# Kernel tuning notes

Hardware: AMD Instinct MI355X
Metric: run time of the kernel (lower is better)

The kernel has to match this reference:

```python
import jax
import jax.numpy as jnp
from jax import lax
import numpy as np

B = 65536
T = 1          # forced by x.view(B, -1) feeding Linear(40, 4)
IN = 1260
H = 40
OUT = 4


def setup_inputs() -> dict:
    key = jax.random.key(0)
    ks = jax.random.split(key, 16)
    s = 0.05
    inp = {"x": jax.random.normal(ks[0], (B, T, IN), dtype=jnp.float32)}
    # 3-layer LSTM params, torch gate order (i, f, g, o) stacked along dim 0
    dims_in = [IN, H, H]
    for l in range(3):
        inp[f"W_ih{l}"] = jax.random.normal(ks[1 + 4 * l], (4 * H, dims_in[l]), dtype=jnp.float32) * s
        inp[f"W_hh{l}"] = jax.random.normal(ks[2 + 4 * l], (4 * H, H), dtype=jnp.float32) * s
        inp[f"b_ih{l}"] = jax.random.normal(ks[3 + 4 * l], (4 * H,), dtype=jnp.float32) * s
        inp[f"b_hh{l}"] = jax.random.normal(ks[4 + 4 * l], (4 * H,), dtype=jnp.float32) * s
    inp["W_out"] = jax.random.normal(ks[13], (OUT, H), dtype=jnp.float32) * s
    inp["b_out"] = jax.random.normal(ks[14], (OUT,), dtype=jnp.float32) * s
    return inp


def _lstm_layer(x, W_ih, W_hh, b_ih, b_hh):
    # x: [B, T, D_in] -> [B, T, H]; zero initial (h, c) as in torch default
    b, _, _ = x.shape
    h0 = jnp.zeros((b, H), x.dtype)
    c0 = jnp.zeros((b, H), x.dtype)

    def step(carry, xt):
        h, c = carry
        gates = xt @ W_ih.T + b_ih + h @ W_hh.T + b_hh   # [B, 4H]
        i, f, g, o = jnp.split(gates, 4, axis=-1)
        i = jax.nn.sigmoid(i)
        f = jax.nn.sigmoid(f)
        g = jnp.tanh(g)
        o = jax.nn.sigmoid(o)
        c = f * c + i * g
        h = o * jnp.tanh(c)
        return (h, c), h

    _, ys = lax.scan(step, (h0, c0), jnp.swapaxes(x, 0, 1))  # ys: [T, B, H]
    return jnp.swapaxes(ys, 0, 1)


def reference(x, W_ih0, W_hh0, b_ih0, b_hh0,
              W_ih1, W_hh1, b_ih1, b_hh1,
              W_ih2, W_hh2, b_ih2, b_hh2,
              W_out, b_out):
    h = _lstm_layer(x, W_ih0, W_hh0, b_ih0, b_hh0)
    h = _lstm_layer(h, W_ih1, W_hh1, b_ih1, b_hh1)
    h = _lstm_layer(h, W_ih2, W_hh2, b_ih2, b_hh2)   # [B, T, H]
    flat = h.reshape(h.shape[0], -1)                  # [B, T*H] == [B, 40]
    return flat @ W_out.T + b_out                     # [B, 4]
```

## Files before the change

kernel.cpp:

```cpp
#include <hip/hip_runtime.h>

typedef float f32x4 __attribute__((ext_vector_type(4)));
typedef __bf16 bf16x8 __attribute__((ext_vector_type(8)));
typedef unsigned short u16x4 __attribute__((ext_vector_type(4)));
typedef unsigned int u32x4 __attribute__((ext_vector_type(4)));


__device__ __forceinline__ unsigned short f2bf(float f) {
  unsigned int u = __builtin_bit_cast(unsigned int, f);
  u = (u + 0x7FFFu + ((u >> 16) & 1u)) >> 16;
  return (unsigned short)u;
}
__device__ __forceinline__ float sigm(float v) { return 1.0f / (1.0f + __expf(-v)); }
__device__ __forceinline__ float tanh_(float v) { return 1.0f - 2.0f / (__expf(2.0f * v) + 1.0f); }

__device__ __forceinline__ int srow_of(int col) {
  return col + (col < 40 ? 0 : (col < 80 ? 40 : 80));
}

__global__ __launch_bounds__(256) void prep_kernel(
    const float* __restrict__ W_ih0, const float* __restrict__ b_ih0, const float* __restrict__ b_hh0,
    const float* __restrict__ W_ih1, const float* __restrict__ b_ih1, const float* __restrict__ b_hh1,
    const float* __restrict__ W_ih2, const float* __restrict__ b_ih2, const float* __restrict__ b_hh2,
    unsigned short* __restrict__ W0bf, unsigned short* __restrict__ W1bf,
    unsigned short* __restrict__ W2bf, float* __restrict__ bias)
{
  int idx = blockIdx.x * 256 + threadIdx.x;
  {
    int c = idx >> 13, rem = idx & 8191;
    int col = rem >> 6, kk = rem & 63;
    int k = (c << 6) + kk;
    unsigned short v = 0;
    if (col < 120 && k < 1260) v = f2bf(W_ih0[srow_of(col) * 1260 + k]);
    W0bf[(c << 13) + (col << 6) + (kk ^ ((col & 7) << 3))] = v;
  }
  if (idx < 8192) {
    int col = idx >> 6, kk = idx & 63;
    unsigned short v1 = 0, v2 = 0;
    if (col < 120 && kk < 40) {
      int sr = srow_of(col);
      v1 = f2bf(W_ih1[sr * 40 + kk]);
      v2 = f2bf(W_ih2[sr * 40 + kk]);
    }
    int d = (col << 6) + (kk ^ ((col & 7) << 3));
    W1bf[d] = v1;
    W2bf[d] = v2;
  }
  if (idx < 384) {
    int l = idx >> 7, col = idx & 127;
    float v = 0.0f;
    if (col < 120) {
      int sr = srow_of(col);
      v = (l == 0) ? (b_ih0[sr] + b_hh0[sr])
        : (l == 1) ? (b_ih1[sr] + b_hh1[sr])
                   : (b_ih2[sr] + b_hh2[sr]);
    }
    bias[idx] = v;
  }
}

__global__ __launch_bounds__(256, 2) void lstm_main(
    const float* __restrict__ x,
    const unsigned short* __restrict__ W0bf,
    const unsigned short* __restrict__ W1bf,
    const unsigned short* __restrict__ W2bf,
    const float* __restrict__ bias,
    const float* __restrict__ W_out,
    const float* __restrict__ b_out,
    float* __restrict__ out)
{
  __shared__ __align__(16) unsigned short Abuf[2][64 * 64];
  __shared__ __align__(16) unsigned short Wbuf[2][128 * 64];
  __shared__ __align__(16) float gates[64 * 124];

  const int tid = threadIdx.x;
  const int wave = tid >> 6;
  const int lane = tid & 63;
  const int l15 = lane & 15;
  const int l4 = lane >> 4;
  const long base_row = (long)blockIdx.x * 64;

  const int arow = tid >> 4;
  const int akq = tid & 15;
  const float* xbase = x + (base_row + arow) * 1260 + akq * 4;

  f32x4 acc[4][2];
  f32x4 areg[4];
  u32x4 wreg[4];
  const f32x4 zero4 = {0.0f, 0.0f, 0.0f, 0.0f};

  auto zacc = [&]() {
#pragma unroll
    for (int i = 0; i < 4; ++i)
#pragma unroll
      for (int j = 0; j < 2; ++j) acc[i][j] = zero4;
  };

  auto loadA = [&](int c) {
    int kg = (c << 6) + (akq << 2);
    bool v = (kg < 1257);
#pragma unroll
    for (int p = 0; p < 4; ++p) {
      const float* s = xbase + p * (16 * 1260) + (c << 6);
      areg[p] = v ? *(const f32x4*)s : zero4;
    }
  };

  auto storeA = [&](int b) {
#pragma unroll
    for (int p = 0; p < 4; ++p) {
      int row = (p << 4) + arow;
      int kk0 = akq << 2;
      int sidx = (row << 6) + (kk0 ^ ((row & 7) << 3));
      u16x4 pk;
      pk.x = f2bf(areg[p].x); pk.y = f2bf(areg[p].y);
      pk.z = f2bf(areg[p].z); pk.w = f2bf(areg[p].w);
      *(u16x4*)&Abuf[b][sidx] = pk;
    }
  };

  auto loadW = [&](const unsigned short* src) {
    const u32x4* ws = (const u32x4*)src;
#pragma unroll
    for (int j = 0; j < 4; ++j) wreg[j] = ws[j * 256 + tid];
  };

  auto storeW = [&](int b) {
    u32x4* wd = (u32x4*)&Wbuf[b][0];
#pragma unroll
    for (int j = 0; j < 4; ++j) wd[j * 256 + tid] = wreg[j];
  };

  auto compute = [&](int b) {
#pragma unroll
    for (int ks = 0; ks < 2; ++ks) {
      bf16x8 af[4], wf[2];
      int kk = (ks << 5) + (l4 << 3);
#pragma unroll
      for (int mt = 0; mt < 4; ++mt) {
        int row = (mt << 4) + l15;
        af[mt] = *(const bf16x8*)&Abuf[b][(row << 6) + (kk ^ ((row & 7) << 3))];
      }
#pragma unroll
      for (int ct = 0; ct < 2; ++ct) {
        int col = (wave << 5) + (ct << 4) + l15;
        wf[ct] = *(const bf16x8*)&Wbuf[b][(col << 6) + (kk ^ ((col & 7) << 3))];
      }
#pragma unroll
      for (int mt = 0; mt < 4; ++mt)
#pragma unroll
        for (int ct = 0; ct < 2; ++ct)
          acc[mt][ct] = __builtin_amdgcn_mfma_f32_16x16x32_bf16(af[mt], wf[ct], acc[mt][ct], 0, 0, 0);
    }
  };

  auto writegates = [&](const float* bp) {
#pragma unroll
    for (int ct = 0; ct < 2; ++ct) {
      int col = (wave << 5) + (ct << 4) + l15;
      if (col < 120) {
        float bv = bp[col];
#pragma unroll
        for (int mt = 0; mt < 4; ++mt) {
          int row = (mt << 4) + (l4 << 2);
#pragma unroll
          for (int r = 0; r < 4; ++r)
            gates[(row + r) * 124 + col] = acc[mt][ct][r] + bv;
        }
      }
    }
  };

  auto zeroA0 = [&]() {
    unsigned int* az = (unsigned int*)&Abuf[0][0];
#pragma unroll
    for (int j = 0; j < 8; ++j) az[j * 256 + tid] = 0u;
  };

  auto act_bf = [&]() {
#pragma unroll
    for (int it = 0; it < 10; ++it) {
      int idx = it * 256 + tid;
      int row = idx / 40;
      int h = idx - row * 40;
      const float* gr = &gates[row * 124];
      float i = sigm(gr[h]);
      float g = tanh_(gr[40 + h]);
      float o = sigm(gr[80 + h]);
      float hv = o * tanh_(i * g);
      Abuf[0][(row << 6) + (h ^ ((row & 7) << 3))] = f2bf(hv);
    }
  };

  zacc();
  loadA(0); loadW(W0bf);
  storeA(0); storeW(0);
  __syncthreads();
  for (int c = 0; c < 20; ++c) {
    int cur = c & 1;
    if (c < 19) { loadA(c + 1); loadW(W0bf + ((long)(c + 1) << 13)); }
    compute(cur);
    if (c < 19) { storeA(cur ^ 1); storeW(cur ^ 1); }
    __syncthreads();
  }

  writegates(bias);
  zeroA0();
  loadW(W1bf);
  __syncthreads();

  act_bf();
  storeW(0);
  __syncthreads();

  zacc();
  compute(0);
  __syncthreads();

  writegates(bias + 128);
  zeroA0();
  loadW(W2bf);
  __syncthreads();

  act_bf();
  storeW(0);
  __syncthreads();

  zacc();
  compute(0);
  __syncthreads();

  writegates(bias + 256);
  __syncthreads();

#pragma unroll
  for (int it = 0; it < 10; ++it) {
    int idx = it * 256 + tid;
    int row = idx / 40;
    int h = idx - row * 40;
    float* gr = &gates[row * 124];
    float i = sigm(gr[h]);
    float g = tanh_(gr[40 + h]);
    float o = sigm(gr[80 + h]);
    gr[h] = o * tanh_(i * g);
  }
  __syncthreads();

  {
    int row = tid >> 2, oi = tid & 3;
    const float* wo = W_out + oi * 40;
    float s = b_out[oi];
    const float* hr = &gates[row * 124];
#pragma unroll
    for (int h = 0; h < 40; ++h) s = fmaf(wo[h], hr[h], s);
    out[(base_row + row) * 4 + oi] = s;
  }
}

extern "C" void kernel_launch(void* const* d_in, const int* in_sizes, int n_in,
                              void* d_out, int out_size, void* d_ws, size_t ws_size,
                              hipStream_t stream) {
  const float* x     = (const float*)d_in[0];
  const float* W_ih0 = (const float*)d_in[1];
  const float* b_ih0 = (const float*)d_in[3];
  const float* b_hh0 = (const float*)d_in[4];
  const float* W_ih1 = (const float*)d_in[5];
  const float* b_ih1 = (const float*)d_in[7];
  const float* b_hh1 = (const float*)d_in[8];
  const float* W_ih2 = (const float*)d_in[9];
  const float* b_ih2 = (const float*)d_in[11];
  const float* b_hh2 = (const float*)d_in[12];
  const float* W_out = (const float*)d_in[13];
  const float* b_out = (const float*)d_in[14];

  unsigned short* W0bf = (unsigned short*)d_ws;
  unsigned short* W1bf = W0bf + 163840;
  unsigned short* W2bf = W1bf + 8192;
  float* bias = (float*)(W2bf + 8192);

  if (ws_size < (size_t)(163840 + 8192 + 8192) * 2 + 384 * 4) return;

  prep_kernel<<<640, 256, 0, stream>>>(W_ih0, b_ih0, b_hh0,
                                       W_ih1, b_ih1, b_hh1,
                                       W_ih2, b_ih2, b_hh2,
                                       W0bf, W1bf, W2bf, bias);
  lstm_main<<<1024, 256, 0, stream>>>(x, W0bf, W1bf, W2bf, bias, W_out, b_out, (float*)d_out);
}
```

Baseline: 480.2 us.

## Restructure LSTM kernel to per-wave register-direct MFMA without shared staging or block barriers

Each wave now owns 16 batch rows and computes all 128 gate columns. It loads x straight from global into MFMA fragments, and weights come from a prepacked fragment-order layout read directly from global/L2, so the shared-memory double buffering and block-wide barriers are gone. The weight prep kernel is changed to emit this fragment-major layout. Occupancy hint is raised to 4 blocks/SM. In exchange, weights are re-read per wave from cache instead of shared once per block, and the x loads are less coalesced (16 rows × 32B segments per fragment).

```diff
diff --git a/kernel.cpp b/kernel.cpp
--- a/kernel.cpp
+++ b/kernel.cpp
@@ -2,8 +2,7 @@
 
 typedef float f32x4 __attribute__((ext_vector_type(4)));
 typedef __bf16 bf16x8 __attribute__((ext_vector_type(8)));
-typedef unsigned short u16x4 __attribute__((ext_vector_type(4)));
-typedef unsigned int u32x4 __attribute__((ext_vector_type(4)));
+typedef unsigned short u16x8 __attribute__((ext_vector_type(8)));
 
 
 __device__ __forceinline__ unsigned short f2bf(float f) {
@@ -22,29 +21,28 @@
     const float* __restrict__ W_ih0, const float* __restrict__ b_ih0, const float* __restrict__ b_hh0,
     const float* __restrict__ W_ih1, const float* __restrict__ b_ih1, const float* __restrict__ b_hh1,
     const float* __restrict__ W_ih2, const float* __restrict__ b_ih2, const float* __restrict__ b_hh2,
-    unsigned short* __restrict__ W0bf, unsigned short* __restrict__ W1bf,
-    unsigned short* __restrict__ W2bf, float* __restrict__ bias)
+    unsigned short* __restrict__ W0f, unsigned short* __restrict__ W1f,
+    unsigned short* __restrict__ W2f, float* __restrict__ bias)
 {
   int idx = blockIdx.x * 256 + threadIdx.x;
   {
-    int c = idx >> 13, rem = idx & 8191;
-    int col = rem >> 6, kk = rem & 63;
-    int k = (c << 6) + kk;
+    int j = idx & 7, col = (idx >> 3) & 127, l4 = (idx >> 10) & 3, ks = (idx >> 12) & 1, c = idx >> 13;
+    int k = c * 64 + ks * 32 + l4 * 8 + j;
     unsigned short v = 0;
     if (col < 120 && k < 1260) v = f2bf(W_ih0[srow_of(col) * 1260 + k]);
-    W0bf[(c << 13) + (col << 6) + (kk ^ ((col & 7) << 3))] = v;
+    W0f[idx] = v;
   }
   if (idx < 8192) {
-    int col = idx >> 6, kk = idx & 63;
+    int j = idx & 7, col = (idx >> 3) & 127, l4 = (idx >> 10) & 3, ks = idx >> 12;
+    int k = ks * 32 + l4 * 8 + j;
     unsigned short v1 = 0, v2 = 0;
-    if (col < 120 && kk < 40) {
+    if (col < 120 && k < 40) {
       int sr = srow_of(col);
-      v1 = f2bf(W_ih1[sr * 40 + kk]);
-      v2 = f2bf(W_ih2[sr * 40 + kk]);
-    }
-    int d = (col << 6) + (kk ^ ((col & 7) << 3));
-    W1bf[d] = v1;
-    W2bf[d] = v2;
+      v1 = f2bf(W_ih1[sr * 40 + k]);
+      v2 = f2bf(W_ih2[sr * 40 + k]);
+    }
+    W1f[idx] = v1;
+    W2f[idx] = v2;
   }
   if (idx < 384) {
     int l = idx >> 7, col = idx & 127;
@@ -59,201 +57,166 @@
   }
 }
 
-__global__ __launch_bounds__(256, 2) void lstm_main(
+__global__ __launch_bounds__(256, 4) void lstm_main(
     const float* __restrict__ x,
-    const unsigned short* __restrict__ W0bf,
-    const unsigned short* __restrict__ W1bf,
-    const unsigned short* __restrict__ W2bf,
+    const unsigned short* __restrict__ W0f,
+    const unsigned short* __restrict__ W1f,
+    const unsigned short* __restrict__ W2f,
     const float* __restrict__ bias,
     const float* __restrict__ W_out,
     const float* __restrict__ b_out,
     float* __restrict__ out)
 {
-  __shared__ __align__(16) unsigned short Abuf[2][64 * 64];
-  __shared__ __align__(16) unsigned short Wbuf[2][128 * 64];
-  __shared__ __align__(16) float gates[64 * 124];
+  __shared__ __align__(16) float gbuf[4][16 * 124];
+  __shared__ __align__(16) unsigned short hbuf[4][16 * 64];
 
   const int tid = threadIdx.x;
   const int wave = tid >> 6;
   const int lane = tid & 63;
   const int l15 = lane & 15;
   const int l4 = lane >> 4;
-  const long base_row = (long)blockIdx.x * 64;
-
-  const int arow = tid >> 4;
-  const int akq = tid & 15;
-  const float* xbase = x + (base_row + arow) * 1260 + akq * 4;
-
-  f32x4 acc[4][2];
-  f32x4 areg[4];
-  u32x4 wreg[4];
-  const f32x4 zero4 = {0.0f, 0.0f, 0.0f, 0.0f};
-
-  auto zacc = [&]() {
-#pragma unroll
-    for (int i = 0; i < 4; ++i)
-#pragma unroll
-      for (int j = 0; j < 2; ++j) acc[i][j] = zero4;
-  };
-
-  auto loadA = [&](int c) {
-    int kg = (c << 6) + (akq << 2);
-    bool v = (kg < 1257);
-#pragma unroll
-    for (int p = 0; p < 4; ++p) {
-      const float* s = xbase + p * (16 * 1260) + (c << 6);
-      areg[p] = v ? *(const f32x4*)s : zero4;
-    }
-  };
-
-  auto storeA = [&](int b) {
-#pragma unroll
-    for (int p = 0; p < 4; ++p) {
-      int row = (p << 4) + arow;
-      int kk0 = akq << 2;
-      int sidx = (row << 6) + (kk0 ^ ((row & 7) << 3));
-      u16x4 pk;
-      pk.x = f2bf(areg[p].x); pk.y = f2bf(areg[p].y);
-      pk.z = f2bf(areg[p].z); pk.w = f2bf(areg[p].w);
-      *(u16x4*)&Abuf[b][sidx] = pk;
-    }
-  };
-
-  auto loadW = [&](const unsigned short* src) {
-    const u32x4* ws = (const u32x4*)src;
-#pragma unroll
-    for (int j = 0; j < 4; ++j) wreg[j] = ws[j * 256 + tid];
-  };
-
-  auto storeW = [&](int b) {
-    u32x4* wd = (u32x4*)&Wbuf[b][0];
-#pragma unroll
-    for (int j = 0; j < 4; ++j) wd[j * 256 + tid] = wreg[j];
-  };
-
-  auto compute = [&](int b) {
+  const long R = (long)blockIdx.x * 64 + wave * 16;
+
+  float* gw = gbuf[wave];
+  unsigned short* hw = hbuf[wave];
+
+#pragma unroll
+  for (int it = 0; it < 6; ++it) {
+    int idx = it * 64 + lane;
+    int row = idx / 24;
+    int kk = 40 + (idx - row * 24);
+    int byte = row * 128 + ((kk * 2) ^ ((row & 7) << 4));
+    *(unsigned short*)((char*)hw + byte) = 0;
+  }
+
+  f32x4 acc[8];
+#pragma unroll
+  for (int i = 0; i < 8; ++i) acc[i] = (f32x4){0.0f, 0.0f, 0.0f, 0.0f};
+
+  auto cvt8 = [](f32x4 a0, f32x4 a1) -> bf16x8 {
+    u16x8 u;
+#pragma unroll
+    for (int j = 0; j < 4; ++j) { u[j] = f2bf(a0[j]); u[4 + j] = f2bf(a1[j]); }
+    return __builtin_bit_cast(bf16x8, u);
+  };
+
+  const float* xp = x + (R + l15) * 1260 + l4 * 8;
+  const unsigned short* wp = W0f + l4 * 1024 + l15 * 8;
+
+#pragma unroll 2
+  for (int c = 0; c < 19; ++c) {
 #pragma unroll
     for (int ks = 0; ks < 2; ++ks) {
-      bf16x8 af[4], wf[2];
-      int kk = (ks << 5) + (l4 << 3);
-#pragma unroll
-      for (int mt = 0; mt < 4; ++mt) {
-        int row = (mt << 4) + l15;
-        af[mt] = *(const bf16x8*)&Abuf[b][(row << 6) + (kk ^ ((row & 7) << 3))];
+      f32x4 a0 = *(const f32x4*)(xp + ks * 32);
+      f32x4 a1 = *(const f32x4*)(xp + ks * 32 + 4);
+      bf16x8 af = cvt8(a0, a1);
+      const unsigned short* wq = wp + ks * 4096;
+#pragma unroll
+      for (int ct = 0; ct < 8; ++ct) {
+        bf16x8 wf = *(const bf16x8*)(wq + ct * 128);
+        acc[ct] = __builtin_amdgcn_mfma_f32_16x16x32_bf16(af, wf, acc[ct], 0, 0, 0);
       }
-#pragma unroll
-      for (int ct = 0; ct < 2; ++ct) {
-        int col = (wave << 5) + (ct << 4) + l15;
-        wf[ct] = *(const bf16x8*)&Wbuf[b][(col << 6) + (kk ^ ((col & 7) << 3))];
-      }
-#pragma unroll
-      for (int mt = 0; mt < 4; ++mt)
-#pragma unroll
-        for (int ct = 0; ct < 2; ++ct)
-          acc[mt][ct] = __builtin_amdgcn_mfma_f32_16x16x32_bf16(af[mt], wf[ct], acc[mt][ct], 0, 0, 0);
-    }
-  };
-
-  auto writegates = [&](const float* bp) {
-#pragma unroll
-    for (int ct = 0; ct < 2; ++ct) {
-      int col = (wave << 5) + (ct << 4) + l15;
+    }
+    xp += 64;
+    wp += 8192;
+  }
+  {
+    const f32x4 z = {0.0f, 0.0f, 0.0f, 0.0f};
+    {
+      f32x4 a0 = *(const f32x4*)(xp);
+      f32x4 a1 = *(const f32x4*)(xp + 4);
+      bf16x8 af = cvt8(a0, a1);
+#pragma unroll
+      for (int ct = 0; ct < 8; ++ct)
+        acc[ct] = __builtin_amdgcn_mfma_f32_16x16x32_bf16(af, *(const bf16x8*)(wp + ct * 128), acc[ct], 0, 0, 0);
+    }
+    {
+      f32x4 a0 = (l4 < 2) ? *(const f32x4*)(xp + 32) : z;
+      f32x4 a1 = (l4 < 1) ? *(const f32x4*)(xp + 36) : z;
+      bf16x8 af = cvt8(a0, a1);
+#pragma unroll
+      for (int ct = 0; ct < 8; ++ct)
+        acc[ct] = __builtin_amdgcn_mfma_f32_16x16x32_bf16(af, *(const bf16x8*)(wp + 4096 + ct * 128), acc[ct], 0, 0, 0);
+    }
+  }
+
+  auto store_gates = [&](const float* bp) {
+#pragma unroll
+    for (int ct = 0; ct < 8; ++ct) {
+      int col = ct * 16 + l15;
       if (col < 120) {
         float bv = bp[col];
 #pragma unroll
-        for (int mt = 0; mt < 4; ++mt) {
-          int row = (mt << 4) + (l4 << 2);
-#pragma unroll
-          for (int r = 0; r < 4; ++r)
-            gates[(row + r) * 124 + col] = acc[mt][ct][r] + bv;
-        }
+        for (int r = 0; r < 4; ++r)
+          gw[(l4 * 4 + r) * 124 + col] = acc[ct][r] + bv;
       }
     }
   };
 
-  auto zeroA0 = [&]() {
-    unsigned int* az = (unsigned int*)&Abuf[0][0];
-#pragma unroll
-    for (int j = 0; j < 8; ++j) az[j * 256 + tid] = 0u;
-  };
-
-  auto act_bf = [&]() {
+  auto act_store = [&]() {
 #pragma unroll
     for (int it = 0; it < 10; ++it) {
-      int idx = it * 256 + tid;
+      int idx = it * 64 + lane;
       int row = idx / 40;
       int h = idx - row * 40;
-      const float* gr = &gates[row * 124];
+      const float* gr = gw + row * 124;
       float i = sigm(gr[h]);
       float g = tanh_(gr[40 + h]);
       float o = sigm(gr[80 + h]);
       float hv = o * tanh_(i * g);
-      Abuf[0][(row << 6) + (h ^ ((row & 7) << 3))] = f2bf(hv);
-    }
-  };
-
-  zacc();
-  loadA(0); loadW(W0bf);
-  storeA(0); storeW(0);
-  __syncthreads();
-  for (int c = 0; c < 20; ++c) {
-    int cur = c & 1;
-    if (c < 19) { loadA(c + 1); loadW(W0bf + ((long)(c + 1) << 13)); }
-    compute(cur);
-    if (c < 19) { storeA(cur ^ 1); storeW(cur ^ 1); }
-    __syncthreads();
-  }
-
-  writegates(bias);
-  zeroA0();
-  loadW(W1bf);
-  __syncthreads();
-
-  act_bf();
-  storeW(0);
-  __syncthreads();
-
-  zacc();
-  compute(0);
-  __syncthreads();
-
-  writegates(bias + 128);
-  zeroA0();
-  loadW(W2bf);
-  __syncthreads();
-
-  act_bf();
-  storeW(0);
-  __syncthreads();
-
-  zacc();
-  compute(0);
-  __syncthreads();
-
-  writegates(bias + 256);
-  __syncthreads();
+      int byte = row * 128 + ((h * 2) ^ ((row & 7) << 4));
+      *(unsigned short*)((char*)hw + byte) = f2bf(hv);
+    }
+  };
+
+  auto small_gemm = [&](const unsigned short* Wf) {
+#pragma unroll
+    for (int ks = 0; ks < 2; ++ks) {
+      int byte = l15 * 128 + (((ks * 32 + l4 * 8) * 2) ^ ((l15 & 7) << 4));
+      bf16x8 af = *(const bf16x8*)((const char*)hw + byte);
+      const unsigned short* wq = Wf + ks * 4096 + l4 * 1024 + l15 * 8;
+#pragma unroll
+      for (int ct = 0; ct < 8; ++ct) {
+        bf16x8 wf = *(const bf16x8*)(wq + ct * 128);
+        acc[ct] = __builtin_amdgcn_mfma_f32_16x16x32_bf16(af, wf, acc[ct], 0, 0, 0);
+      }
+    }
+  };
+
+  store_gates(bias);
+  act_store();
+
+#pragma unroll
+  for (int i = 0; i < 8; ++i) acc[i] = (f32x4){0.0f, 0.0f, 0.0f, 0.0f};
+  small_gemm(W1f);
+  store_gates(bias + 128);
+  act_store();
+
+#pragma unroll
+  for (int i = 0; i < 8; ++i) acc[i] = (f32x4){0.0f, 0.0f, 0.0f, 0.0f};
+  small_gemm(W2f);
+  store_gates(bias + 256);
 
 #pragma unroll
   for (int it = 0; it < 10; ++it) {
-    int idx = it * 256 + tid;
+    int idx = it * 64 + lane;
     int row = idx / 40;
     int h = idx - row * 40;
-    float* gr = &gates[row * 124];
+    float* gr = gw + row * 124;
     float i = sigm(gr[h]);
     float g = tanh_(gr[40 + h]);
     float o = sigm(gr[80 + h]);
     gr[h] = o * tanh_(i * g);
   }
-  __syncthreads();
 
   {
-    int row = tid >> 2, oi = tid & 3;
+    int row = lane >> 2, oi = lane & 3;
     const float* wo = W_out + oi * 40;
     float s = b_out[oi];
-    const float* hr = &gates[row * 124];
+    const float* hr = gw + row * 124;
 #pragma unroll
     for (int h = 0; h < 40; ++h) s = fmaf(wo[h], hr[h], s);
-    out[(base_row + row) * 4 + oi] = s;
+    out[(R + row) * 4 + oi] = s;
   }
 }
 
@@ -273,16 +236,16 @@
   const float* W_out = (const float*)d_in[13];
   const float* b_out = (const float*)d_in[14];
 
-  unsigned short* W0bf = (unsigned short*)d_ws;
-  unsigned short* W1bf = W0bf + 163840;
-  unsigned short* W2bf = W1bf + 8192;
-  float* bias = (float*)(W2bf + 8192);
+  unsigned short* W0f = (unsigned short*)d_ws;
+  unsigned short* W1f = W0f + 163840;
+  unsigned short* W2f = W1f + 8192;
+  float* bias = (float*)(W2f + 8192);
 
   if (ws_size < (size_t)(163840 + 8192 + 8192) * 2 + 384 * 4) return;
 
   prep_kernel<<<640, 256, 0, stream>>>(W_ih0, b_ih0, b_hh0,
                                        W_ih1, b_ih1, b_hh1,
                                        W_ih2, b_ih2, b_hh2,
-                                       W0bf, W1bf, W2bf, bias);
-  lstm_main<<<1024, 256, 0, stream>>>(x, W0bf, W1bf, W2bf, bias, W_out, b_out, (float*)d_out);
-}
+                                       W0f, W1f, W2f, bias);
+  lstm_main<<<1024, 256, 0, stream>>>(x, W0f, W1f, W2f, bias, W_out, b_out, (float*)d_out);
+}
```

Result: slower. 524.3 us (+9.2%).
